# Optimization experiments

Measured on AMD Instinct MI355X. Metric: run time of the kernel, lower is better.

The kernel has to match this reference:

```python
import jax, jax.numpy as jnp
import numpy as np

N_NODES = 50000
N_EDGES = 800000
D = 128          # input_node_dim == output_node_dim (residual)
T = 3            # number of node types == number of edge types
NODE_IN = D + T * D  # node updater input dim = 512


def setup_inputs() -> dict:
    key = jax.random.key(0)
    ks = jax.random.split(key, 8)
    scale = 0.05
    return {
        "node_feature": jax.random.normal(ks[0], (N_NODES, D), jnp.float32),
        "W_e": jax.random.normal(ks[1], (T, D, D), jnp.float32) * scale,
        "b_e": jnp.zeros((T, D), jnp.float32),
        "W_n": jax.random.normal(ks[2], (T, D, NODE_IN), jnp.float32) * scale,
        "b_n": jnp.zeros((T, D), jnp.float32),
        "edge_src": jax.random.randint(ks[3], (N_EDGES,), 0, N_NODES, jnp.int32),
        "edge_dst": jax.random.randint(ks[4], (N_EDGES,), 0, N_NODES, jnp.int32),
        "edge_type": jax.random.randint(ks[5], (N_EDGES,), 0, T, jnp.int32),
        "node_type": jax.random.randint(ks[6], (N_NODES,), 0, T, jnp.int32),
    }


def reference(node_feature, W_e, b_e, W_n, b_n, edge_src, edge_dst, edge_type, node_type):
    N, Din = node_feature.shape
    n_types = W_e.shape[0]
    out_dim = W_e.shape[1]

    # message_function: per-edge-type MLP on source features, relu, zero elsewhere
    src = node_feature[edge_src]                      # [E, D] gather
    parts = [jax.nn.relu(node_feature)]               # reduce_function relu's node_feature
    for t in range(n_types):
        msg = jax.nn.relu(src @ W_e[t].T + b_e[t])    # [E, out]
        msg = jnp.where((edge_type == t)[:, None], msg, jnp.zeros((), msg.dtype))
        # mailbox sum over incoming edges per destination node
        parts.append(jax.ops.segment_sum(msg, edge_dst, num_segments=N))
    agg = jnp.concatenate(parts, axis=1)              # [N, D + T*out]

    # per-node-type updater MLP, dispatched by node_type
    updated = jnp.zeros((N, out_dim), node_feature.dtype)
    for t in range(n_types):
        o = agg @ W_n[t].T + b_n[t]                   # [N, out]
        updated = jnp.where((node_type == t)[:, None], o, updated)

    # use_residual = True
    return updated + node_feature
```

## Files before the change

kernel.cpp:

```cpp
#include <hip/hip_runtime.h>
#include <hip/hip_bf16.h>

#define NN 50000
#define NE 800000
#define DD 128
#define NT 3
#define AGGW 384
#define EM 64
#define EM2 128
#define LDK 136
#define CB 32
#define LDK2 520
#define NBITS 7
#define NBINS ((NN + 127) / 128)
#define EPB 2048
#define BINCAP 2560
#define NTILES_MAX (((NN + EM - 1) / EM) + NT)
#define NTILE_PAD (((NTILES_MAX + 7) / 8) * 8)

typedef __bf16 bf16x8 __attribute__((ext_vector_type(8)));
typedef float f32x4 __attribute__((ext_vector_type(4)));
typedef unsigned short u16x8 __attribute__((ext_vector_type(8)));
typedef unsigned int u32x4 __attribute__((ext_vector_type(4)));

__device__ __forceinline__ unsigned short f2b(float f) {
    __hip_bfloat16 h = __float2bfloat16(f);
    return __builtin_bit_cast(unsigned short, h);
}
__device__ __forceinline__ float b2f(unsigned int u16bits) {
    unsigned int x = u16bits << 16;
    return __builtin_bit_cast(float, x);
}

__global__ void k_prep(const float* __restrict__ nf, const float* __restrict__ We,
                       const float* __restrict__ Wn, unsigned short* __restrict__ nfb,
                       unsigned short* __restrict__ Web, unsigned short* __restrict__ Wnb,
                       int* __restrict__ bhist, int* __restrict__ cnts) {
    size_t i = (size_t)blockIdx.x * blockDim.x + threadIdx.x;
    if (i < NBINS) bhist[i] = 0;
    if (i >= NBINS && i < NBINS + 16) cnts[i - NBINS] = 0;
    const size_t n0 = (size_t)NN * DD / 8;
    const size_t n1 = (size_t)NT * DD * DD / 8;
    const size_t n2 = (size_t)NT * DD * 512 / 8;
    size_t total = n0 + n1 + n2;
    for (size_t p = i; p < total; p += (size_t)gridDim.x * blockDim.x) {
        const float* s; unsigned short* d; size_t off;
        if (p < n0)            { s = nf; d = nfb; off = p; }
        else if (p < n0 + n1)  { s = We; d = Web; off = p - n0; }
        else                   { s = Wn; d = Wnb; off = p - n0 - n1; }
        const float4* f4 = (const float4*)(s + off * 8);
        float4 x = f4[0], y = f4[1];
        u16x8 u = { f2b(x.x), f2b(x.y), f2b(x.z), f2b(x.w),
                    f2b(y.x), f2b(y.y), f2b(y.z), f2b(y.w) };
        *(u16x8*)(d + off * 8) = u;
    }
}

__global__ __launch_bounds__(256) void k_binhist(const int* __restrict__ edst,
        const int* __restrict__ ntp, int* __restrict__ bhist, int* __restrict__ cnts) {
    __shared__ int lh[NBINS];
    __shared__ int ln[3];
    int tid = threadIdx.x;
    for (int i = tid; i < NBINS; i += 256) lh[i] = 0;
    if (tid < 3) ln[tid] = 0;
    __syncthreads();
    int i0 = blockIdx.x * blockDim.x + tid;
    int stride = gridDim.x * blockDim.x;
    for (int p = i0; p < NE; p += stride) atomicAdd(&lh[edst[p] >> NBITS], 1);
    for (int p = i0; p < NN; p += stride) atomicAdd(&ln[ntp[p]], 1);
    __syncthreads();
    for (int i = tid; i < NBINS; i += 256) if (lh[i]) atomicAdd(&bhist[i], lh[i]);
    if (tid < 3) atomicAdd(&cnts[6 + tid], ln[tid]);
}

__global__ __launch_bounds__(512) void k_binscan(const int* __restrict__ bhist,
        int* __restrict__ binptr, int* __restrict__ bincur, int* __restrict__ rowptr) {
    __shared__ int sa[NBINS], sb[NBINS];
    int tid = threadIdx.x;
    if (tid < NBINS) sa[tid] = bhist[tid];
    __syncthreads();
    int flip = 0;
    for (int off = 1; off < NBINS; off <<= 1) {
        int* src = flip ? sb : sa;
        int* dst = flip ? sa : sb;
        if (tid < NBINS) dst[tid] = src[tid] + ((tid >= off) ? src[tid - off] : 0);
        __syncthreads();
        flip ^= 1;
    }
    int* inc = flip ? sb : sa;
    if (tid < NBINS) {
        int excl = (tid == 0) ? 0 : inc[tid - 1];
        binptr[tid] = excl;
        bincur[tid] = excl;
    }
    if (tid == 0) { binptr[NBINS] = NE; rowptr[NN] = NE; }
}

__global__ __launch_bounds__(512) void k_mid(
        const unsigned short* __restrict__ nfb, const unsigned short* __restrict__ Web,
        const float* __restrict__ be, unsigned short* __restrict__ M,
        const int* __restrict__ esrc, const int* __restrict__ edst,
        const int* __restrict__ et, const int* __restrict__ ntp,
        int* __restrict__ bincur, int* __restrict__ cnts,
        int* __restrict__ pe, int* __restrict__ sn) {
    const int NEB = (NE + EPB - 1) / EPB;
    const int NCH2 = (NN + 511) / 512;
    const int TILES = (NN + EM2 - 1) / EM2;
    __shared__ unsigned short Wsm[DD][LDK];
    int tid = threadIdx.x, b = blockIdx.x;

    if (b < NEB) {
        int* lh = (int*)&Wsm[0][0];
        int* gb = lh + NBINS;
        int* lr = gb + NBINS;
        for (int i = tid; i < NBINS; i += 512) { lh[i] = 0; lr[i] = 0; }
        __syncthreads();
        int e0 = b * EPB;
#pragma unroll
        for (int i = 0; i < EPB; i += 512) {
            int e = e0 + i + tid;
            if (e < NE) atomicAdd(&lh[edst[e] >> NBITS], 1);
        }
        __syncthreads();
        for (int i = tid; i < NBINS; i += 512)
            if (lh[i]) gb[i] = atomicAdd(&bincur[i], lh[i]);
        __syncthreads();
#pragma unroll
        for (int i = 0; i < EPB; i += 512) {
            int e = e0 + i + tid;
            if (e < NE) {
                int d = edst[e];
                int t = et[e];
                int bin = d >> NBITS;
                int rank = atomicAdd(&lr[bin], 1);
                pe[gb[bin] + rank] = (t * NN + esrc[e]) | ((d & 127) << 18) | (t << 25);
            }
        }
    } else if (b < NEB + NCH2) {
        int* lcnt = (int*)&Wsm[0][0];
        int* lbase = lcnt + 4;
        if (tid < 3) lcnt[tid] = 0;
        __syncthreads();
        int p = (b - NEB) * 512 + tid;
        int t = -1, rank = 0;
        if (p < NN) { t = ntp[p]; rank = atomicAdd(&lcnt[t], 1); }
        __syncthreads();
        if (tid < 3) lbase[tid] = atomicAdd(&cnts[9 + tid], lcnt[tid]);
        __syncthreads();
        if (p < NN) {
            int c0 = cnts[6], c1 = cnts[7];
            int off = (t == 0) ? 0 : (t == 1) ? c0 : c0 + c1;
            sn[off + lbase[t] + rank] = p;
        }
    } else {
        int bb = b - NEB - NCH2;
        int t = bb / TILES, tile = bb % TILES;
        int base = tile * EM2;
        int m = min(EM2, NN - base);
        {
            int row = tid >> 2, c0 = (tid & 3) * 32;
            const u16x8* src = (const u16x8*)(Web + ((size_t)t * DD + row) * DD + c0);
#pragma unroll
            for (int v = 0; v < 4; ++v) *(u16x8*)&Wsm[row][c0 + v * 8] = src[v];
        }
        __syncthreads();

        int wave = tid >> 6, l = tid & 63, lr2 = l & 15, kg = l >> 4;
        int arow = min(base + wave * 16 + lr2, NN - 1);
        const u16x8* Arow = (const u16x8*)(nfb + (size_t)arow * DD);
        f32x4 acc[8];
#pragma unroll
        for (int n = 0; n < 8; n++) acc[n] = (f32x4){0.f, 0.f, 0.f, 0.f};
#pragma unroll
        for (int k0 = 0; k0 < DD; k0 += 32) {
            bf16x8 a = __builtin_bit_cast(bf16x8, Arow[(k0 >> 3) + kg]);
#pragma unroll
            for (int n = 0; n < 8; n++) {
                bf16x8 bbv = *(const bf16x8*)&Wsm[n * 16 + lr2][k0 + kg * 8];
                acc[n] = __builtin_amdgcn_mfma_f32_16x16x32_bf16(a, bbv, acc[n], 0, 0, 0);
            }
        }
        unsigned short* Mt = M + (size_t)t * NN * DD;
#pragma unroll
        for (int n = 0; n < 8; n++) {
            int col = n * 16 + lr2;
            float bias = be[t * DD + col];
#pragma unroll
            for (int r = 0; r < 4; r++) {
                int row = wave * 16 + kg * 4 + r;
                if (row < m) {
                    float v = acc[n][r] + bias;
                    Mt[(size_t)(base + row) * DD + col] = f2b(fmaxf(v, 0.f));
                }
            }
        }
    }
}

__global__ __launch_bounds__(256) void k_binsort(const int* __restrict__ binptr,
        int* __restrict__ pe, int* __restrict__ rowptr) {
    __shared__ int lcnt[128], lrk[128], lrp[128];
    __shared__ unsigned int sorted[BINCAP];
    int b = blockIdx.x, tid = threadIdx.x;
    int beg = binptr[b], end = binptr[b + 1];
    int cnt = min(end - beg, BINCAP);
    if (tid < 128) { lcnt[tid] = 0; lrk[tid] = 0; }
    __syncthreads();
    for (int e = tid; e < cnt; e += 256)
        atomicAdd(&lcnt[(pe[beg + e] >> 18) & 127], 1);
    __syncthreads();
    if (tid < 64) {
        int v = lcnt[2 * tid] + lcnt[2 * tid + 1];
        int s = v;
        for (int d = 1; d < 64; d <<= 1) {
            int u = __shfl_up(s, d);
            if (tid >= d) s += u;
        }
        int excl = s - v;
        lrp[2 * tid] = excl;
        lrp[2 * tid + 1] = excl + lcnt[2 * tid];
    }
    __syncthreads();
    if (tid < 128) {
        int node = b * 128 + tid;
        if (node < NN) rowptr[node] = beg + lrp[tid];
    }
    for (int e = tid; e < cnt; e += 256) {
        unsigned int p = pe[beg + e];
        int d = (p >> 18) & 127;
        int pos = lrp[d] + atomicAdd(&lrk[d], 1);
        sorted[pos] = p;
    }
    __syncthreads();
    for (int e = tid; e < cnt; e += 256) pe[beg + e] = sorted[e];
}

__global__ __launch_bounds__(128) void k_agg(const unsigned short* __restrict__ M,
        const int* __restrict__ rowptr, const int* __restrict__ pe,
        unsigned short* __restrict__ aggb) {
    int node = blockIdx.x * 8 + (threadIdx.x >> 4);
    int q = threadIdx.x & 15;
    int beg = rowptr[node], end = rowptr[node + 1];
    const u32x4* Mu4 = (const u32x4*)M;
    float a0[8] = {0,0,0,0,0,0,0,0};
    float a1[8] = {0,0,0,0,0,0,0,0};
    float a2[8] = {0,0,0,0,0,0,0,0};
    int e = beg;
    while (e < end) {
        unsigned int p[8];
        u32x4 v[8];
#pragma unroll
        for (int j = 0; j < 8; ++j) p[j] = pe[min(e + j, end - 1)];
#pragma unroll
        for (int j = 0; j < 8; ++j)
            if (e + j < end) v[j] = Mu4[(size_t)(p[j] & 0x3FFFFu) * 16 + q];
#pragma unroll
        for (int j = 0; j < 8; ++j) {
            if (e + j < end) {
                int t = p[j] >> 25;
                float f0 = b2f(v[j][0] & 0xFFFF), f1 = b2f(v[j][0] >> 16);
                float f2 = b2f(v[j][1] & 0xFFFF), f3 = b2f(v[j][1] >> 16);
                float f4 = b2f(v[j][2] & 0xFFFF), f5 = b2f(v[j][2] >> 16);
                float f6 = b2f(v[j][3] & 0xFFFF), f7 = b2f(v[j][3] >> 16);
                if (t == 0) {
                    a0[0] += f0; a0[1] += f1; a0[2] += f2; a0[3] += f3;
                    a0[4] += f4; a0[5] += f5; a0[6] += f6; a0[7] += f7;
                } else if (t == 1) {
                    a1[0] += f0; a1[1] += f1; a1[2] += f2; a1[3] += f3;
                    a1[4] += f4; a1[5] += f5; a1[6] += f6; a1[7] += f7;
                } else {
                    a2[0] += f0; a2[1] += f1; a2[2] += f2; a2[3] += f3;
                    a2[4] += f4; a2[5] += f5; a2[6] += f6; a2[7] += f7;
                }
            }
        }
        e += 8;
    }
    unsigned int* dst = (unsigned int*)(aggb + (size_t)node * AGGW);
    u32x4 o0 = { (unsigned int)f2b(a0[0]) | ((unsigned int)f2b(a0[1]) << 16),
                 (unsigned int)f2b(a0[2]) | ((unsigned int)f2b(a0[3]) << 16),
                 (unsigned int)f2b(a0[4]) | ((unsigned int)f2b(a0[5]) << 16),
                 (unsigned int)f2b(a0[6]) | ((unsigned int)f2b(a0[7]) << 16) };
    u32x4 o1 = { (unsigned int)f2b(a1[0]) | ((unsigned int)f2b(a1[1]) << 16),
                 (unsigned int)f2b(a1[2]) | ((unsigned int)f2b(a1[3]) << 16),
                 (unsigned int)f2b(a1[4]) | ((unsigned int)f2b(a1[5]) << 16),
                 (unsigned int)f2b(a1[6]) | ((unsigned int)f2b(a1[7]) << 16) };
    u32x4 o2 = { (unsigned int)f2b(a2[0]) | ((unsigned int)f2b(a2[1]) << 16),
                 (unsigned int)f2b(a2[2]) | ((unsigned int)f2b(a2[3]) << 16),
                 (unsigned int)f2b(a2[4]) | ((unsigned int)f2b(a2[5]) << 16),
                 (unsigned int)f2b(a2[6]) | ((unsigned int)f2b(a2[7]) << 16) };
    ((u32x4*)dst)[q]        = o0;
    ((u32x4*)(dst + 64))[q] = o1;
    ((u32x4*)(dst + 128))[q] = o2;
}

__global__ __launch_bounds__(256, 3) void k_node(const float* __restrict__ nf,
        const unsigned short* __restrict__ nfb, const unsigned short* __restrict__ Wnb,
        const float* __restrict__ bn, const int* __restrict__ sn,
        const int* __restrict__ cnts, const unsigned short* __restrict__ aggb,
        float* __restrict__ out) {
    __shared__ unsigned short Wsm[CB][LDK2];
    int c0 = cnts[6], c1 = cnts[7], c2 = cnts[8];
    int n0 = (c0 + EM - 1) / EM, n1 = (c1 + EM - 1) / EM, n2 = (c2 + EM - 1) / EM;
    int ntile = n0 + n1 + n2;
    int b = blockIdx.x;
    int rt = (b & 7) * (NTILE_PAD / 8) + (b >> 3);
    if (rt >= ntile) return;
    int tid = threadIdx.x;
    int wave = tid >> 6, l = tid & 63, lr = l & 15, kg = l >> 4;
    int t, tile;
    if (rt < n0) { t = 0; tile = rt; }
    else if (rt < n0 + n1) { t = 1; tile = rt - n0; }
    else { t = 2; tile = rt - n0 - n1; }
    int off = (t == 0) ? 0 : (t == 1) ? c0 : c0 + c1;
    int cntt = (t == 0) ? c0 : (t == 1) ? c1 : c2;
    int base = off + tile * EM;
    int m = min(EM, cntt - tile * EM);

    int myrow = sn[base + min(wave * 16 + lr, m - 1)];
    const u16x8* An = (const u16x8*)(nfb + (size_t)myrow * DD);
    const u16x8* Ag = (const u16x8*)(aggb + (size_t)myrow * AGGW);
    u16x8 afr[16];
#pragma unroll
    for (int kc = 0; kc < 4; ++kc) {
#pragma unroll
        for (int k0 = 0; k0 < DD; k0 += 32) {
            u16x8 araw;
            if (kc == 0) {
                araw = An[(k0 >> 3) + kg];
#pragma unroll
                for (int j = 0; j < 8; ++j)
                    araw[j] = (araw[j] & 0x8000) ? (unsigned short)0 : araw[j];
            } else {
                araw = Ag[((kc - 1) * DD + k0) / 8 + kg];
            }
            afr[kc * 4 + (k0 >> 5)] = araw;
        }
    }

    int nd[4];
#pragma unroll
    for (int r = 0; r < 4; ++r) nd[r] = sn[base + min(wave * 16 + kg * 4 + r, m - 1)];

    int srow = tid & 31, scc = (tid >> 5) * 64;
#pragma unroll 1
    for (int cbk = 0; cbk < 4; ++cbk) {
        if (cbk) __syncthreads();
        const u16x8* src = (const u16x8*)(Wnb + ((size_t)t * DD + cbk * CB + srow) * 512 + scc);
#pragma unroll
        for (int v = 0; v < 8; ++v) *(u16x8*)&Wsm[srow][scc + v * 8] = src[v];
        __syncthreads();

        f32x4 acc0 = {0.f, 0.f, 0.f, 0.f}, acc1 = {0.f, 0.f, 0.f, 0.f};
#pragma unroll
        for (int kc = 0; kc < 4; ++kc) {
#pragma unroll
            for (int k0 = 0; k0 < DD; k0 += 32) {
                bf16x8 a = __builtin_bit_cast(bf16x8, afr[kc * 4 + (k0 >> 5)]);
                int kw = kc * DD + k0 + kg * 8;
                bf16x8 b0 = *(const bf16x8*)&Wsm[lr][kw];
                bf16x8 b1 = *(const bf16x8*)&Wsm[16 + lr][kw];
                acc0 = __builtin_amdgcn_mfma_f32_16x16x32_bf16(a, b0, acc0, 0, 0, 0);
                acc1 = __builtin_amdgcn_mfma_f32_16x16x32_bf16(a, b1, acc1, 0, 0, 0);
            }
        }
#pragma unroll
        for (int n = 0; n < 2; n++) {
            int col = cbk * CB + n * 16 + lr;
            float bias = bn[t * DD + col];
            const f32x4& av = n ? acc1 : acc0;
#pragma unroll
            for (int r = 0; r < 4; r++) {
                int row = wave * 16 + kg * 4 + r;
                if (row < m) {
                    int node = nd[r];
                    out[(size_t)node * DD + col] = av[r] + bias + nf[(size_t)node * DD + col];
                }
            }
        }
    }
}

extern "C" void kernel_launch(void* const* d_in, const int* in_sizes, int n_in,
                              void* d_out, int out_size, void* d_ws, size_t ws_size,
                              hipStream_t stream) {
    const float* nf   = (const float*)d_in[0];
    const float* We   = (const float*)d_in[1];
    const float* be   = (const float*)d_in[2];
    const float* Wn   = (const float*)d_in[3];
    const float* bn   = (const float*)d_in[4];
    const int*   esrc = (const int*)d_in[5];
    const int*   edst = (const int*)d_in[6];
    const int*   et   = (const int*)d_in[7];
    const int*   ntp  = (const int*)d_in[8];
    float* out = (float*)d_out;

    char* w = (char*)d_ws;
    unsigned short* M    = (unsigned short*)w;  w += (size_t)NT * NN * DD * 2;
    unsigned short* aggb = (unsigned short*)w;  w += (size_t)NN * AGGW * 2;
    unsigned short* nfb  = (unsigned short*)w;  w += (size_t)NN * DD * 2;
    unsigned short* Web  = (unsigned short*)w;  w += (size_t)NT * DD * DD * 2;
    unsigned short* Wnb  = (unsigned short*)w;  w += (size_t)NT * DD * 512 * 2;
    int* pe     = (int*)w;  w += (size_t)NE * 4;
    int* bhist  = (int*)w;  w += (NBINS + 1) * 4;
    int* binptr = (int*)w;  w += (NBINS + 1) * 4;
    int* bincur = (int*)w;  w += (NBINS + 1) * 4;
    int* rowptr = (int*)w;  w += (size_t)(NN + 1) * 4;
    int* sn     = (int*)w;  w += (size_t)NN * 4;
    int* cnts   = (int*)w;  w += 16 * 4;

    const int NEB = (NE + EPB - 1) / EPB;
    const int NCH2 = (NN + 511) / 512;
    const int TILES2 = (NN + EM2 - 1) / EM2;

    k_prep<<<1024, 256, 0, stream>>>(nf, We, Wn, nfb, Web, Wnb, bhist, cnts);
    k_binhist<<<256, 256, 0, stream>>>(edst, ntp, bhist, cnts);
    k_binscan<<<1, 512, 0, stream>>>(bhist, binptr, bincur, rowptr);
    k_mid<<<NEB + NCH2 + NT * TILES2, 512, 0, stream>>>(nfb, Web, be, M,
            esrc, edst, et, ntp, bincur, cnts, pe, sn);
    k_binsort<<<NBINS, 256, 0, stream>>>(binptr, pe, rowptr);
    k_agg<<<NN / 8, 128, 0, stream>>>(M, rowptr, pe, aggb);
    k_node<<<NTILE_PAD, 256, 0, stream>>>(nf, nfb, Wnb, bn, sn, cnts, aggb, out);
}
```

Before: 138.1 us.

## Store aggregates in type-sorted order and use per-wave bin histograms

k_agg now writes each node's aggregated row at its position in the node-type-sorted order, using a new rank array built during node bucketing. k_node can then read aggregate rows contiguously instead of gathering them by node id. Separately, the edge binning pass uses per-wave local histograms with a prefix across waves, which reduces LDS atomic contention on the shared bin counters. The cost is an extra rank array, an indirect store in k_agg, and more shared memory for the histograms.

```diff
diff --git a/kernel.cpp b/kernel.cpp
--- a/kernel.cpp
+++ b/kernel.cpp
@@ -17,6 +17,7 @@
 #define BINCAP 2560
 #define NTILES_MAX (((NN + EM - 1) / EM) + NT)
 #define NTILE_PAD (((NTILES_MAX + 7) / 8) * 8)
+#define LHS 392
 
 typedef __bf16 bf16x8 __attribute__((ext_vector_type(8)));
 typedef float f32x4 __attribute__((ext_vector_type(4)));
@@ -102,7 +103,7 @@
         const int* __restrict__ esrc, const int* __restrict__ edst,
         const int* __restrict__ et, const int* __restrict__ ntp,
         int* __restrict__ bincur, int* __restrict__ cnts,
-        int* __restrict__ pe, int* __restrict__ sn) {
+        int* __restrict__ pe, int* __restrict__ sn, int* __restrict__ rnk) {
     const int NEB = (NE + EPB - 1) / EPB;
     const int NCH2 = (NN + 511) / 512;
     const int TILES = (NN + EM2 - 1) / EM2;
@@ -111,29 +112,34 @@
 
     if (b < NEB) {
         int* lh = (int*)&Wsm[0][0];
-        int* gb = lh + NBINS;
-        int* lr = gb + NBINS;
-        for (int i = tid; i < NBINS; i += 512) { lh[i] = 0; lr[i] = 0; }
-        __syncthreads();
-        int e0 = b * EPB;
-#pragma unroll
-        for (int i = 0; i < EPB; i += 512) {
-            int e = e0 + i + tid;
-            if (e < NE) atomicAdd(&lh[edst[e] >> NBITS], 1);
-        }
-        __syncthreads();
-        for (int i = tid; i < NBINS; i += 512)
-            if (lh[i]) gb[i] = atomicAdd(&bincur[i], lh[i]);
-        __syncthreads();
-#pragma unroll
-        for (int i = 0; i < EPB; i += 512) {
-            int e = e0 + i + tid;
+        int* lr = lh + 8 * LHS;
+        int* gb = lr + 8 * LHS;
+        int wv = tid >> 6, ln = tid & 63;
+        for (int i = tid; i < 8 * LHS; i += 512) { lh[i] = 0; lr[i] = 0; }
+        __syncthreads();
+        int ew0 = b * EPB + wv * 256;
+#pragma unroll
+        for (int i = 0; i < 256; i += 64) {
+            int e = ew0 + i + ln;
+            if (e < NE) atomicAdd(&lh[wv * LHS + (edst[e] >> NBITS)], 1);
+        }
+        __syncthreads();
+        for (int i = tid; i < NBINS; i += 512) {
+            int s = 0;
+#pragma unroll
+            for (int w = 0; w < 8; ++w) { int t = lh[w * LHS + i]; lh[w * LHS + i] = s; s += t; }
+            if (s) gb[i] = atomicAdd(&bincur[i], s);
+        }
+        __syncthreads();
+#pragma unroll
+        for (int i = 0; i < 256; i += 64) {
+            int e = ew0 + i + ln;
             if (e < NE) {
                 int d = edst[e];
                 int t = et[e];
                 int bin = d >> NBITS;
-                int rank = atomicAdd(&lr[bin], 1);
-                pe[gb[bin] + rank] = (t * NN + esrc[e]) | ((d & 127) << 18) | (t << 25);
+                int pos = gb[bin] + lh[wv * LHS + bin] + atomicAdd(&lr[wv * LHS + bin], 1);
+                pe[pos] = (t * NN + esrc[e]) | ((d & 127) << 18) | (t << 25);
             }
         }
     } else if (b < NEB + NCH2) {
@@ -150,7 +156,9 @@
         if (p < NN) {
             int c0 = cnts[6], c1 = cnts[7];
             int off = (t == 0) ? 0 : (t == 1) ? c0 : c0 + c1;
-            sn[off + lbase[t] + rank] = p;
+            int pos = off + lbase[t] + rank;
+            sn[pos] = p;
+            rnk[p] = pos;
         }
     } else {
         int bb = b - NEB - NCH2;
@@ -237,7 +245,7 @@
 
 __global__ __launch_bounds__(128) void k_agg(const unsigned short* __restrict__ M,
         const int* __restrict__ rowptr, const int* __restrict__ pe,
-        unsigned short* __restrict__ aggb) {
+        const int* __restrict__ rnk, unsigned short* __restrict__ aggb) {
     int node = blockIdx.x * 8 + (threadIdx.x >> 4);
     int q = threadIdx.x & 15;
     int beg = rowptr[node], end = rowptr[node + 1];
@@ -276,7 +284,7 @@
         }
         e += 8;
     }
-    unsigned int* dst = (unsigned int*)(aggb + (size_t)node * AGGW);
+    unsigned int* dst = (unsigned int*)(aggb + (size_t)rnk[node] * AGGW);
     u32x4 o0 = { (unsigned int)f2b(a0[0]) | ((unsigned int)f2b(a0[1]) << 16),
                  (unsigned int)f2b(a0[2]) | ((unsigned int)f2b(a0[3]) << 16),
                  (unsigned int)f2b(a0[4]) | ((unsigned int)f2b(a0[5]) << 16),
@@ -317,9 +325,10 @@
     int base = off + tile * EM;
     int m = min(EM, cntt - tile * EM);
 
-    int myrow = sn[base + min(wave * 16 + lr, m - 1)];
+    int srtrow = base + min(wave * 16 + lr, m - 1);
+    int myrow = sn[srtrow];
     const u16x8* An = (const u16x8*)(nfb + (size_t)myrow * DD);
-    const u16x8* Ag = (const u16x8*)(aggb + (size_t)myrow * AGGW);
+    const u16x8* Ag = (const u16x8*)(aggb + (size_t)srtrow * AGGW);
     u16x8 afr[16];
 #pragma unroll
     for (int kc = 0; kc < 4; ++kc) {
@@ -407,6 +416,7 @@
     int* bincur = (int*)w;  w += (NBINS + 1) * 4;
     int* rowptr = (int*)w;  w += (size_t)(NN + 1) * 4;
     int* sn     = (int*)w;  w += (size_t)NN * 4;
+    int* rnk    = (int*)w;  w += (size_t)NN * 4;
     int* cnts   = (int*)w;  w += 16 * 4;
 
     const int NEB = (NE + EPB - 1) / EPB;
@@ -417,8 +427,8 @@
     k_binhist<<<256, 256, 0, stream>>>(edst, ntp, bhist, cnts);
     k_binscan<<<1, 512, 0, stream>>>(bhist, binptr, bincur, rowptr);
     k_mid<<<NEB + NCH2 + NT * TILES2, 512, 0, stream>>>(nfb, Web, be, M,
-            esrc, edst, et, ntp, bincur, cnts, pe, sn);
+            esrc, edst, et, ntp, bincur, cnts, pe, sn, rnk);
     k_binsort<<<NBINS, 256, 0, stream>>>(binptr, pe, rowptr);
-    k_agg<<<NN / 8, 128, 0, stream>>>(M, rowptr, pe, aggb);
+    k_agg<<<NN / 8, 128, 0, stream>>>(M, rowptr, pe, rnk, aggb);
     k_node<<<NTILE_PAD, 256, 0, stream>>>(nf, nfb, Wnb, bn, sn, cnts, aggb, out);
 }
```

Result: no change. 138.3 us (+0.2%).
